# Performance work log

Hardware: AMD Instinct MI355X
Metric: run time of the kernel (lower is better)

## Reference

```python
import jax, jax.numpy as jnp
import numpy as np

N = 50000      # num nodes (genes)
E = 800000     # num edges (TF->Target)
IN = 128       # in_channels
HID = 16       # hidden_channels per head
HEADS = 4
OUT = 32       # out_channels
NEG_SLOPE = 0.2  # PyG GATConv leaky_relu slope
EPS = 1e-16


def setup_inputs() -> dict:
    key = jax.random.key(0)
    ks = jax.random.split(key, 11)
    x = jax.random.normal(ks[0], (N, IN), dtype=jnp.float32)
    edge_index = jax.random.randint(ks[1], (2, E), 0, N, dtype=jnp.int32)
    # layer 1: heads=HEADS, concat=True
    W1 = jax.random.normal(ks[2], (IN, HEADS * HID), dtype=jnp.float32) * (1.0 / np.sqrt(IN))
    a_src1 = jax.random.normal(ks[3], (HEADS, HID), dtype=jnp.float32) * 0.1
    a_dst1 = jax.random.normal(ks[4], (HEADS, HID), dtype=jnp.float32) * 0.1
    b1 = jnp.zeros((HEADS * HID,), dtype=jnp.float32)
    # layer 2: heads=1, concat=False
    W2 = jax.random.normal(ks[5], (HEADS * HID, OUT), dtype=jnp.float32) * (1.0 / np.sqrt(HEADS * HID))
    a_src2 = jax.random.normal(ks[6], (1, OUT), dtype=jnp.float32) * 0.1
    a_dst2 = jax.random.normal(ks[7], (1, OUT), dtype=jnp.float32) * 0.1
    b2 = jnp.zeros((OUT,), dtype=jnp.float32)
    return dict(x=x, edge_index=edge_index, W1=W1, a_src1=a_src1, a_dst1=a_dst1, b1=b1,
                W2=W2, a_src2=a_src2, a_dst2=a_dst2, b2=b2)


def gat_layer(x, edge_index, W, a_src, a_dst, b, concat):
    """PyG GATConv (no self-loops, eval mode): gather -> edge attention -> segment softmax -> scatter."""
    n = x.shape[0]
    heads, ch = a_src.shape
    h = (x @ W).reshape(n, heads, ch)                      # [N, H, C]
    alpha_s = jnp.einsum('nhc,hc->nh', h, a_src)           # [N, H]
    alpha_d = jnp.einsum('nhc,hc->nh', h, a_dst)           # [N, H]
    src, dst = edge_index[0], edge_index[1]
    e = jax.nn.leaky_relu(alpha_s[src] + alpha_d[dst], negative_slope=NEG_SLOPE)  # [E, H]
    # numerically stable softmax over incoming edges of each dst node
    m = jax.ops.segment_max(e, dst, num_segments=n)        # [N, H]
    e = jnp.exp(e - m[dst])
    denom = jax.ops.segment_sum(e, dst, num_segments=n)    # [N, H]
    alpha = e / (denom[dst] + EPS)                         # [E, H]
    msg = h[src] * alpha[:, :, None]                       # [E, H, C]
    out = jax.ops.segment_sum(msg, dst, num_segments=n)    # [N, H, C]
    if concat:
        out = out.reshape(n, heads * ch)
    else:
        out = out.mean(axis=1)
    return out + b


def reference(x, edge_index, W1, a_src1, a_dst1, b1, W2, a_src2, a_dst2, b2):
    h = gat_layer(x, edge_index, W1, a_src1, a_dst1, b1, concat=True)   # [N, HEADS*HID]
    h = jax.nn.elu(h)
    out = gat_layer(h, edge_index, W2, a_src2, a_dst2, b2, concat=False)  # [N, OUT]
    return out
```

## Files before the change

### kernel.cpp

```cpp
#include <hip/hip_runtime.h>
#include <math.h>

#define NN 50000
#define NE 800000
#define INCH 128
#define HID1 16
#define H1 4
#define C1 64
#define C2 32
#define NEG 0.2f
#define EPSF 1e-16f
#define BSH 7
#define NBKT 391
#define CAPB 3072
#define EPB 2048
#define NPB1 391
#define GB1 782

static __device__ __forceinline__ float lrelu(float v){ return v > 0.f ? v : NEG * v; }


__global__ __launch_bounds__(256) void k_part1(const int* __restrict__ ei, int* bcnt,
                                               int2* __restrict__ pairs){
    __shared__ int hist[512];
    __shared__ int scn[512];
    __shared__ int spos[512];
    __shared__ int gbase[NBKT];
    __shared__ int2 stg[EPB];
    int t = threadIdx.x;
    hist[t] = 0; hist[t + 256] = 0;
    __syncthreads();

    int e0 = blockIdx.x * EPB;
    int tot = NE - e0; if (tot > EPB) tot = EPB;
    int srcv[8], dstv[8], rnk[8], bkt[8];
    #pragma unroll
    for (int k = 0; k < 8; ++k){
        int idx = k * 256 + t;
        if (idx < tot){
            int e = e0 + idx;
            srcv[k] = ei[e];
            dstv[k] = ei[NE + e];
            bkt[k] = dstv[k] >> BSH;
            rnk[k] = atomicAdd(&hist[bkt[k]], 1);
        } else bkt[k] = -1;
    }
    __syncthreads();

    int* sA = hist; int* sB = scn;
    for (int off = 1; off < 512; off <<= 1){
        int v0 = sA[t]       + ((t       >= off) ? sA[t - off]       : 0);
        int v1 = sA[t + 256] + ((t + 256 >= off) ? sA[t + 256 - off] : 0);
        __syncthreads();
        sB[t] = v0; sB[t + 256] = v1;
        __syncthreads();
        int* tmp = sA; sA = sB; sB = tmp;
    }
    for (int b = t; b < NBKT; b += 256){
        int incl = sA[b];
        int excl = (b > 0) ? sA[b - 1] : 0;
        spos[b] = excl;
        int cnt = incl - excl;
        gbase[b] = (cnt > 0) ? atomicAdd(&bcnt[b], cnt) : 0;
    }
    __syncthreads();

    #pragma unroll
    for (int k = 0; k < 8; ++k)
        if (bkt[k] >= 0){
            int2 pr; pr.x = srcv[k]; pr.y = dstv[k];
            stg[spos[bkt[k]] + rnk[k]] = pr;
        }
    __syncthreads();

    for (int i = t; i < tot; i += 256){
        int2 pr = stg[i];
        int b = pr.y >> BSH;
        pairs[(size_t)b * CAPB + gbase[b] + (i - spos[b])] = pr;
    }
}


__global__ __launch_bounds__(256) void k_build2(
        const int2* __restrict__ pairs, const int* __restrict__ bcnt,
        int* __restrict__ rows, int* __restrict__ deg, int* __restrict__ srcs,
        const float* __restrict__ x, const float* __restrict__ W,
        const float* __restrict__ asrc, const float* __restrict__ adst,
        float* __restrict__ h, float* __restrict__ as1, float* __restrict__ ad1){
    __shared__ __align__(16) char smem[76288];
    int t = threadIdx.x;

    if (blockIdx.x < NBKT){
        int2* stg = (int2*)smem;
        int* hist = (int*)(smem + 24576);
        int* scn  = (int*)(smem + 25088);
        int* cur  = (int*)(smem + 25600);
        int b = blockIdx.x;
        int n0 = b << BSH;
        int cnt = bcnt[b];
        if (t < 128) hist[t] = 0;
        __syncthreads();
        const int2* psrc = pairs + (size_t)b * CAPB;
        for (int i = t; i < cnt; i += 256){
            int2 pr = psrc[i];
            stg[i] = pr;
            atomicAdd(&hist[pr.y - n0], 1);
        }
        __syncthreads();
        int v = (t < 128) ? hist[t] : 0;
        if (t < 128) scn[t] = v;
        __syncthreads();
        for (int off = 1; off < 128; off <<= 1){
            int add = (t < 128 && t >= off) ? scn[t - off] : 0;
            __syncthreads();
            if (t < 128) scn[t] += add;
            __syncthreads();
        }
        if (t < 128){
            int base = b * CAPB + (scn[t] - v);
            cur[t] = base;
            int n = n0 + t;
            if (n < NN){ rows[n] = base; deg[n] = v; }
        }
        __syncthreads();
        for (int i = t; i < cnt; i += 256){
            int2 pr = stg[i];
            int p = atomicAdd(&cur[pr.y - n0], 1);
            srcs[p] = pr.x;
        }
    } else {
        float (*XT)[68] = (float(*)[68])smem;
        float* WS = (float*)(smem + 34816);
        float (*ps)[17] = (float(*)[17])(smem + 67584);
        float (*pd)[17] = (float(*)[17])(smem + 71936);
        int bid = blockIdx.x - NBKT;

        int nodeL = t >> 2;
        int kc = t & 3;
        int g = bid * 64 + nodeL;
        int gc = min(g, NN - 1);
        const float4* xr = (const float4*)(x + (size_t)gc * INCH);
        #pragma unroll
        for (int i = 0; i < 8; ++i){
            int k = kc * 32 + i * 4;
            float4 v = xr[k >> 2];
            XT[k + 0][nodeL] = v.x;
            XT[k + 1][nodeL] = v.y;
            XT[k + 2][nodeL] = v.z;
            XT[k + 3][nodeL] = v.w;
        }
        const float4* W4 = (const float4*)W;
        float4* WS4 = (float4*)WS;
        #pragma unroll
        for (int i = 0; i < 8; ++i) WS4[i * 256 + t] = W4[i * 256 + t];
        __syncthreads();

        int tx = t & 15, ty = t >> 4;
        int c4 = tx * 4, n4 = ty * 4;
        float acc[4][4];
        #pragma unroll
        for (int a = 0; a < 4; ++a)
            #pragma unroll
            for (int b2 = 0; b2 < 4; ++b2) acc[a][b2] = 0.f;

        #pragma unroll 8
        for (int k = 0; k < INCH; ++k){
            float4 xa = *(const float4*)&XT[k][n4];
            float4 wb = *(const float4*)&WS[k * C1 + c4];
            const float xv[4] = {xa.x, xa.y, xa.z, xa.w};
            const float wv[4] = {wb.x, wb.y, wb.z, wb.w};
            #pragma unroll
            for (int a = 0; a < 4; ++a)
                #pragma unroll
                for (int b2 = 0; b2 < 4; ++b2)
                    acc[a][b2] = fmaf(xv[a], wv[b2], acc[a][b2]);
        }

        int hd = tx >> 2;
        #pragma unroll
        for (int a = 0; a < 4; ++a){
            int n = bid * 64 + n4 + a;
            if (n < NN){
                float4 o = {acc[a][0], acc[a][1], acc[a][2], acc[a][3]};
                *(float4*)&h[(size_t)n * C1 + c4] = o;
            }
            float sa = 0.f, da = 0.f;
            #pragma unroll
            for (int b2 = 0; b2 < 4; ++b2){
                sa = fmaf(acc[a][b2], asrc[hd * HID1 + (c4 & 15) + b2], sa);
                da = fmaf(acc[a][b2], adst[hd * HID1 + (c4 & 15) + b2], da);
            }
            ps[n4 + a][tx] = sa;
            pd[n4 + a][tx] = da;
        }
        __syncthreads();
        int nd = t & 63, hh = t >> 6;
        int g2 = bid * 64 + nd;
        if (g2 < NN){
            float sa = ps[nd][hh*4+0] + ps[nd][hh*4+1] + ps[nd][hh*4+2] + ps[nd][hh*4+3];
            float da = pd[nd][hh*4+0] + pd[nd][hh*4+1] + pd[nd][hh*4+2] + pd[nd][hh*4+3];
            as1[g2 * H1 + hh] = sa;
            ad1[g2 * H1 + hh] = da;
        }
    }
}


__global__ __launch_bounds__(256) void k_aggA(
        const int* __restrict__ srcs, const int* __restrict__ rows,
        const int* __restrict__ deg, const float* __restrict__ h1,
        const float* __restrict__ as, const float* __restrict__ ad,
        const float* __restrict__ b1, const float* __restrict__ W2,
        const float* __restrict__ a2s, const float* __restrict__ a2d,
        float* __restrict__ h2, float* __restrict__ as2, float* __restrict__ ad2){
    __shared__ float hpT[16][65];
    __shared__ float WS[C1 * C2];
    int t = threadIdx.x;
    {
        const float4* W4 = (const float4*)W2;
        float4* WS4 = (float4*)WS;
        WS4[t] = W4[t];
        WS4[256 + t] = W4[256 + t];
    }
    int w = t >> 6, lane = t & 63, hd = lane >> 4;
    float bv = b1[lane];
    #pragma unroll
    for (int q = 0; q < 4; ++q){
        int node = blockIdx.x * 16 + w * 4 + q;
        int start = rows[node], dg = deg[node];
        float adv = ad[node * H1 + hd];
        const float* hL = h1 + lane;
        float ss0 = 0.f, ss1 = 0.f, ac0 = 0.f, ac1 = 0.f, ac2 = 0.f, ac3 = 0.f;
        int j = 0;
        for (; j + 3 < dg; j += 4){
            int s0 = srcs[start + j], s1 = srcs[start + j + 1];
            int s2 = srcs[start + j + 2], s3 = srcs[start + j + 3];
            float w0 = __expf(lrelu(as[s0 * H1 + hd] + adv));
            float w1 = __expf(lrelu(as[s1 * H1 + hd] + adv));
            float w2 = __expf(lrelu(as[s2 * H1 + hd] + adv));
            float w3 = __expf(lrelu(as[s3 * H1 + hd] + adv));
            ss0 += w0 + w2; ss1 += w1 + w3;
            ac0 = fmaf(hL[(size_t)s0 * C1], w0, ac0);
            ac1 = fmaf(hL[(size_t)s1 * C1], w1, ac1);
            ac2 = fmaf(hL[(size_t)s2 * C1], w2, ac2);
            ac3 = fmaf(hL[(size_t)s3 * C1], w3, ac3);
        }
        for (; j < dg; ++j){
            int s = srcs[start + j];
            float wv = __expf(lrelu(as[s * H1 + hd] + adv));
            ss0 += wv;
            ac0 = fmaf(hL[(size_t)s * C1], wv, ac0);
        }
        float o = (ac0 + ac1 + ac2 + ac3) / (ss0 + ss1 + EPSF) + bv;
        hpT[w * 4 + q][lane] = o > 0.f ? o : expm1f(o);
    }
    __syncthreads();

    int n = t >> 4, c = t & 15;
    float a0 = 0.f, a1 = 0.f;
    #pragma unroll 8
    for (int k = 0; k < C1; ++k){
        float hv = hpT[n][k];
        a0 = fmaf(hv, WS[k * C2 + c], a0);
        a1 = fmaf(hv, WS[k * C2 + c + 16], a1);
    }
    int gn = blockIdx.x * 16 + n;
    h2[(size_t)gn * C2 + c] = a0;
    h2[(size_t)gn * C2 + c + 16] = a1;
    float sa = a0 * a2s[c] + a1 * a2s[c + 16];
    float da = a0 * a2d[c] + a1 * a2d[c + 16];
    #pragma unroll
    for (int off = 8; off >= 1; off >>= 1){
        sa += __shfl_xor(sa, off);
        da += __shfl_xor(da, off);
    }
    if (c == 0){ as2[gn] = sa; ad2[gn] = da; }
}


__global__ __launch_bounds__(256) void k_agg2(
        const int* __restrict__ srcs, const int* __restrict__ rows,
        const int* __restrict__ deg, const float* __restrict__ h2,
        const float* __restrict__ as, const float* __restrict__ ad,
        const float* __restrict__ b2, float* __restrict__ out){
    int sl = threadIdx.x >> 5;
    int lane = threadIdx.x & 31;
    int node = blockIdx.x * 8 + sl;
    int start = rows[node], dg = deg[node];
    float adv = ad[node];
    const float* hL = h2 + lane;
    float ss0 = 0.f, ss1 = 0.f, ac0 = 0.f, ac1 = 0.f, ac2 = 0.f, ac3 = 0.f;
    int j = 0;
    for (; j + 3 < dg; j += 4){
        int s0 = srcs[start + j], s1 = srcs[start + j + 1];
        int s2 = srcs[start + j + 2], s3 = srcs[start + j + 3];
        float w0 = __expf(lrelu(as[s0] + adv));
        float w1 = __expf(lrelu(as[s1] + adv));
        float w2 = __expf(lrelu(as[s2] + adv));
        float w3 = __expf(lrelu(as[s3] + adv));
        ss0 += w0 + w2; ss1 += w1 + w3;
        ac0 = fmaf(hL[(size_t)s0 * C2], w0, ac0);
        ac1 = fmaf(hL[(size_t)s1 * C2], w1, ac1);
        ac2 = fmaf(hL[(size_t)s2 * C2], w2, ac2);
        ac3 = fmaf(hL[(size_t)s3 * C2], w3, ac3);
    }
    for (; j < dg; ++j){
        int s = srcs[start + j];
        float wv = __expf(lrelu(as[s] + adv));
        ss0 += wv;
        ac0 = fmaf(hL[(size_t)s * C2], wv, ac0);
    }
    out[(size_t)node * C2 + lane] = (ac0 + ac1 + ac2 + ac3) / (ss0 + ss1 + EPSF) + b2[lane];
}

extern "C" void kernel_launch(void* const* d_in, const int* in_sizes, int n_in,
                              void* d_out, int out_size, void* d_ws, size_t ws_size,
                              hipStream_t stream) {
    const float* x    = (const float*)d_in[0];
    const int*   ei   = (const int*)  d_in[1];
    const float* W1   = (const float*)d_in[2];
    const float* as1w = (const float*)d_in[3];
    const float* ad1w = (const float*)d_in[4];
    const float* b1   = (const float*)d_in[5];
    const float* W2   = (const float*)d_in[6];
    const float* as2w = (const float*)d_in[7];
    const float* ad2w = (const float*)d_in[8];
    const float* b2   = (const float*)d_in[9];
    float* out = (float*)d_out;

    float* p = (float*)d_ws;
    float* h1   = p; p += (size_t)NN * C1;
    float* as1  = p; p += (size_t)NN * H1;
    float* ad1  = p; p += (size_t)NN * H1;
    float* h2   = p; p += (size_t)NN * C2;
    float* as2  = p; p += NN;
    float* ad2  = p; p += NN;
    int* deg  = (int*)p; p += NN;
    int* rows = (int*)p; p += NN;
    int* bcnt = (int*)p; p += NBKT + 57;
    int* srcs = (int*)p; p += (size_t)NBKT * CAPB;
    int2* pairs = (int2*)p;

    dim3 B(256);
    hipMemsetAsync(bcnt, 0, NBKT * sizeof(int), stream);
    k_part1 <<<NPB1, B, 0, stream>>>(ei, bcnt, pairs);
    k_build2<<<NBKT + GB1, B, 0, stream>>>(pairs, bcnt, rows, deg, srcs,
                                           x, W1, as1w, ad1w, h1, as1, ad1);
    k_aggA  <<<NN / 16, B, 0, stream>>>(srcs, rows, deg, h1, as1, ad1, b1,
                                        W2, as2w, ad2w, h2, as2, ad2);
    k_agg2  <<<NN / 8, B, 0, stream>>>(srcs, rows, deg, h2, as2, ad2, b2, out);
}
```

Baseline: 197.5 us.

## Compute edge attention weights cooperatively once into LDS before feature aggregation

Both aggregation kernels now run a first pass in which lanes split the edges of a node. Each lane computes that edge's exp(leaky_relu) weight once and stores it and the source index in shared memory. The old code had every channel lane recompute the same weights redundantly. The second pass reads the weights and indices from LDS to accumulate the gathered features. It keeps a fallback for degrees above 128 and adds LDS use and a dependency through shared memory, with no explicit barrier within the wavefront.

```diff
diff --git a/kernel.cpp b/kernel.cpp
--- a/kernel.cpp
+++ b/kernel.cpp
@@ -10,6 +10,7 @@
 #define C2 32
 #define NEG 0.2f
 #define EPSF 1e-16f
+#define CAP 128
 #define BSH 7
 #define NBKT 391
 #define CAPB 3072
@@ -213,6 +214,9 @@
         const float* __restrict__ b1, const float* __restrict__ W2,
         const float* __restrict__ a2s, const float* __restrict__ a2d,
         float* __restrict__ h2, float* __restrict__ as2, float* __restrict__ ad2){
+    __shared__ float vbuf[4][CAP * H1];
+    __shared__ int   sbuf[4][CAP];
+    __shared__ float sinv[4][4];
     __shared__ float hpT[16][65];
     __shared__ float WS[C1 * C2];
     int t = threadIdx.x;
@@ -222,37 +226,56 @@
         WS4[t] = W4[t];
         WS4[256 + t] = W4[256 + t];
     }
-    int w = t >> 6, lane = t & 63, hd = lane >> 4;
+    int w = t >> 6, lane = t & 63;
+    int hd1 = lane & 3, eb = lane >> 2;
+    int hd3 = lane >> 4;
     float bv = b1[lane];
+
     #pragma unroll
     for (int q = 0; q < 4; ++q){
         int node = blockIdx.x * 16 + w * 4 + q;
         int start = rows[node], dg = deg[node];
-        float adv = ad[node * H1 + hd];
-        const float* hL = h1 + lane;
-        float ss0 = 0.f, ss1 = 0.f, ac0 = 0.f, ac1 = 0.f, ac2 = 0.f, ac3 = 0.f;
-        int j = 0;
-        for (; j + 3 < dg; j += 4){
-            int s0 = srcs[start + j], s1 = srcs[start + j + 1];
-            int s2 = srcs[start + j + 2], s3 = srcs[start + j + 3];
-            float w0 = __expf(lrelu(as[s0 * H1 + hd] + adv));
-            float w1 = __expf(lrelu(as[s1 * H1 + hd] + adv));
-            float w2 = __expf(lrelu(as[s2 * H1 + hd] + adv));
-            float w3 = __expf(lrelu(as[s3 * H1 + hd] + adv));
-            ss0 += w0 + w2; ss1 += w1 + w3;
-            ac0 = fmaf(hL[(size_t)s0 * C1], w0, ac0);
-            ac1 = fmaf(hL[(size_t)s1 * C1], w1, ac1);
-            ac2 = fmaf(hL[(size_t)s2 * C1], w2, ac2);
-            ac3 = fmaf(hL[(size_t)s3 * C1], w3, ac3);
-        }
-        for (; j < dg; ++j){
-            int s = srcs[start + j];
-            float wv = __expf(lrelu(as[s * H1 + hd] + adv));
-            ss0 += wv;
-            ac0 = fmaf(hL[(size_t)s * C1], wv, ac0);
-        }
-        float o = (ac0 + ac1 + ac2 + ac3) / (ss0 + ss1 + EPSF) + bv;
-        hpT[w * 4 + q][lane] = o > 0.f ? o : expm1f(o);
+        if (dg <= CAP){
+            float adv = ad[node * H1 + hd1];
+            float ssum = 0.f;
+            for (int j = eb; j < dg; j += 16){
+                int s = srcs[start + j];
+                float wv = __expf(lrelu(as[s * H1 + hd1] + adv));
+                vbuf[w][j * H1 + hd1] = wv;
+                if (hd1 == 0) sbuf[w][j] = s;
+                ssum += wv;
+            }
+            ssum += __shfl_xor(ssum, 4);
+            ssum += __shfl_xor(ssum, 8);
+            ssum += __shfl_xor(ssum, 16);
+            ssum += __shfl_xor(ssum, 32);
+            if (lane < 4) sinv[w][lane] = 1.f / (ssum + EPSF);
+            float ac0 = 0.f, ac1 = 0.f;
+            const float* hL = h1 + lane;
+            int j = 0;
+            for (; j + 1 < dg; j += 2){
+                int s0 = sbuf[w][j], s1 = sbuf[w][j + 1];
+                float w0 = vbuf[w][j * H1 + hd3], w1 = vbuf[w][(j + 1) * H1 + hd3];
+                ac0 = fmaf(hL[(size_t)s0 * C1], w0, ac0);
+                ac1 = fmaf(hL[(size_t)s1 * C1], w1, ac1);
+            }
+            if (j < dg)
+                ac0 = fmaf(hL[(size_t)sbuf[w][j] * C1], vbuf[w][j * H1 + hd3], ac0);
+            float o = (ac0 + ac1) * sinv[w][hd3] + bv;
+            hpT[w * 4 + q][lane] = o > 0.f ? o : expm1f(o);
+        } else {
+            float adv = ad[node * H1 + hd3];
+            float ss = 0.f, ac = 0.f;
+            const float* hL = h1 + lane;
+            for (int j = 0; j < dg; ++j){
+                int s = srcs[start + j];
+                float wv = __expf(lrelu(as[s * H1 + hd3] + adv));
+                ss += wv;
+                ac = fmaf(hL[(size_t)s * C1], wv, ac);
+            }
+            float o = ac / (ss + EPSF) + bv;
+            hpT[w * 4 + q][lane] = o > 0.f ? o : expm1f(o);
+        }
     }
     __syncthreads();
 
@@ -283,34 +306,49 @@
         const int* __restrict__ deg, const float* __restrict__ h2,
         const float* __restrict__ as, const float* __restrict__ ad,
         const float* __restrict__ b2, float* __restrict__ out){
+    __shared__ float vbuf[8][CAP];
+    __shared__ int   sbuf[8][CAP];
     int sl = threadIdx.x >> 5;
     int lane = threadIdx.x & 31;
     int node = blockIdx.x * 8 + sl;
     int start = rows[node], dg = deg[node];
     float adv = ad[node];
-    const float* hL = h2 + lane;
-    float ss0 = 0.f, ss1 = 0.f, ac0 = 0.f, ac1 = 0.f, ac2 = 0.f, ac3 = 0.f;
-    int j = 0;
-    for (; j + 3 < dg; j += 4){
-        int s0 = srcs[start + j], s1 = srcs[start + j + 1];
-        int s2 = srcs[start + j + 2], s3 = srcs[start + j + 3];
-        float w0 = __expf(lrelu(as[s0] + adv));
-        float w1 = __expf(lrelu(as[s1] + adv));
-        float w2 = __expf(lrelu(as[s2] + adv));
-        float w3 = __expf(lrelu(as[s3] + adv));
-        ss0 += w0 + w2; ss1 += w1 + w3;
-        ac0 = fmaf(hL[(size_t)s0 * C2], w0, ac0);
-        ac1 = fmaf(hL[(size_t)s1 * C2], w1, ac1);
-        ac2 = fmaf(hL[(size_t)s2 * C2], w2, ac2);
-        ac3 = fmaf(hL[(size_t)s3 * C2], w3, ac3);
-    }
-    for (; j < dg; ++j){
-        int s = srcs[start + j];
-        float wv = __expf(lrelu(as[s] + adv));
-        ss0 += wv;
-        ac0 = fmaf(hL[(size_t)s * C2], wv, ac0);
-    }
-    out[(size_t)node * C2 + lane] = (ac0 + ac1 + ac2 + ac3) / (ss0 + ss1 + EPSF) + b2[lane];
+
+    if (dg <= CAP){
+        float ssum = 0.f;
+        for (int j = lane; j < dg; j += 32){
+            int s = srcs[start + j];
+            float wv = __expf(lrelu(as[s] + adv));
+            vbuf[sl][j] = wv;
+            sbuf[sl][j] = s;
+            ssum += wv;
+        }
+        #pragma unroll
+        for (int off = 1; off < 32; off <<= 1) ssum += __shfl_xor(ssum, off);
+        float inv = 1.f / (ssum + EPSF);
+        float ac0 = 0.f, ac1 = 0.f;
+        const float* hL = h2 + lane;
+        int j = 0;
+        for (; j + 1 < dg; j += 2){
+            int s0 = sbuf[sl][j], s1 = sbuf[sl][j + 1];
+            float w0 = vbuf[sl][j], w1 = vbuf[sl][j + 1];
+            ac0 = fmaf(hL[(size_t)s0 * C2], w0, ac0);
+            ac1 = fmaf(hL[(size_t)s1 * C2], w1, ac1);
+        }
+        if (j < dg)
+            ac0 = fmaf(hL[(size_t)sbuf[sl][j] * C2], vbuf[sl][j], ac0);
+        out[(size_t)node * C2 + lane] = (ac0 + ac1) * inv + b2[lane];
+    } else {
+        float ss = 0.f, ac = 0.f;
+        const float* hL = h2 + lane;
+        for (int j = 0; j < dg; ++j){
+            int s = srcs[start + j];
+            float wv = __expf(lrelu(as[s] + adv));
+            ss += wv;
+            ac = fmaf(hL[(size_t)s * C2], wv, ac);
+        }
+        out[(size_t)node * C2 + lane] = ac / (ss + EPSF) + b2[lane];
+    }
 }
 
 extern "C" void kernel_launch(void* const* d_in, const int* in_sizes, int n_in,
```

Measured after the change: 198.8 us. No clear change (+0.7%).
